# Kernel optimization log

Hardware: AMD Instinct MI355X
Metric: run time of the kernel (lower is better)

Reference implementation:

```python
import jax, jax.numpy as jnp
import numpy as np

HEADS = 8

def group_conv1x1(x, w, heads):
    # x: (B, Cin, H, W); w: (Cout, Cin//heads, 1, 1) grouped 1x1 conv, no bias
    B, Cin, H, W = x.shape
    Cout = w.shape[0]
    xg = x.reshape(B, heads, Cin // heads, H * W)
    wg = w[:, :, 0, 0].reshape(heads, Cout // heads, Cin // heads)
    out = jnp.einsum('hoc,bhcl->bhol', wg, xg)
    return out.reshape(B, Cout, H, W)

def sine_pe(d_model, length):
    # standard transformer sin/cos encoding, laid out as (d_model, length)
    pos = jnp.arange(length, dtype=jnp.float32)
    i = jnp.arange(0, d_model, 2, dtype=jnp.float32)
    div = jnp.exp(-(jnp.log(10000.0)) * i / d_model)
    ang = div[:, None] * pos[None, :]            # (d/2, L)
    pe = jnp.zeros((d_model, length), dtype=jnp.float32)
    pe = pe.at[0::2].set(jnp.sin(ang)).at[1::2].set(jnp.cos(ang))
    return pe

def setup_inputs() -> dict:
    key = jax.random.key(0)
    k0, k1, k2, k3 = jax.random.split(key, 4)
    B, Cin, H, W = 16, 256, 32, 32
    Cout, heads = 256, HEADS
    fan_out = Cout  # kaiming_normal fan_out for 1x1 conv = Cout*1*1
    std = np.sqrt(2.0 / fan_out)
    x = jax.random.normal(k0, (B, Cin, H, W), dtype=jnp.float32)
    wq = jax.random.normal(k1, (Cout, Cin // heads, 1, 1), dtype=jnp.float32) * std
    wk = jax.random.normal(k2, (Cout, Cin // heads, 1, 1), dtype=jnp.float32) * std
    wv = jax.random.normal(k3, (Cout, Cin // heads, 1, 1), dtype=jnp.float32) * std
    return {"x": x, "wq": wq, "wk": wk, "wv": wv}

def reference(x, wq, wk, wv):
    B, Cin, H, W = x.shape
    Cout = wq.shape[0]
    heads = HEADS
    dh = Cout // heads
    L = H * W

    q = group_conv1x1(x, wq, heads)              # (B, Cout, H, W)
    k = group_conv1x1(x, wk, heads)
    v = group_conv1x1(x, wv, heads)

    # sine positional encoding added to keys over flattened spatial positions
    k = k.reshape(B, Cout, L) + sine_pe(Cout, L)[None]

    q = q.reshape(B, heads, dh, L)               # (B, h, dh, L)
    k = k.reshape(B, heads, dh, L)
    v = v.reshape(B, heads, dh, L)

    scores = jnp.einsum('bhdq,bhdk->bhqk', q, k)  # (B, h, L, L) -- no sqrt(d) scaling, as in source
    attn = jax.nn.softmax(scores, axis=-1)
    out = jnp.einsum('bhqk,bhdk->bhdq', attn, v)  # (B, h, dh, L)
    return out.reshape(B, Cout, H, W)
```

## Files before the change

### kernel.cpp

```cpp
#include <hip/hip_runtime.h>

#define LL   1024
#define LOG2E 1.44269504088896340736f
#define SMEM_BYTES (131072 + 10240 + 32)

typedef unsigned int       uint;
typedef unsigned short     ushort;
typedef unsigned long long ull;

typedef __attribute__((ext_vector_type(8)))  __bf16          bf16x8;
typedef __attribute__((ext_vector_type(8)))  unsigned short  u16x8;
typedef __attribute__((ext_vector_type(4)))  unsigned short  u16x4;
typedef __attribute__((ext_vector_type(2)))  uint            ui32x2;
typedef __attribute__((ext_vector_type(4)))  uint            ui32x4;
typedef __attribute__((ext_vector_type(4)))  float           f32x4;
typedef __attribute__((ext_vector_type(16))) float           f32x16;

static __device__ __forceinline__ ushort f2bf(float f){
  union {float f; uint u;} v; v.f = f;
  uint u = v.u + 0x7fffu + ((v.u >> 16) & 1u);
  return (ushort)(u >> 16);
}
static __device__ __forceinline__ uint pack2(float a, float b){
  return (uint)f2bf(a) | ((uint)f2bf(b) << 16);
}
static __device__ __forceinline__ uint packtrunc(float a, float b){
  union {float f; uint u;} x, y; x.f = a; y.f = b;
  return __builtin_amdgcn_perm(y.u, x.u, 0x07060302u);
}
static __device__ __forceinline__ bf16x8 ld_frag(const ushort* p){
  u16x8 t = *(const u16x8*)p;
  return __builtin_bit_cast(bf16x8, t);
}
static __device__ __forceinline__ bf16x8 cvt8(const float* p){
  float4 f0 = *(const float4*)p, f1 = *(const float4*)(p + 4);
  u16x8 t;
  t[0]=f2bf(f0.x); t[1]=f2bf(f0.y); t[2]=f2bf(f0.z); t[3]=f2bf(f0.w);
  t[4]=f2bf(f1.x); t[5]=f2bf(f1.y); t[6]=f2bf(f1.z); t[7]=f2bf(f1.w);
  return __builtin_bit_cast(bf16x8, t);
}

static __device__ __forceinline__ void attn_tile(
    f32x16& O, float& rs, bf16x8 q0, bf16x8 q1,
    bf16x8 k00, bf16x8 k01, bf16x8 k10, bf16x8 k11,
    bf16x8 v0, bf16x8 v1, bf16x8 v2, bf16x8 v3, int h)
{
  f32x16 zz = {};
  f32x16 st0 = __builtin_amdgcn_mfma_f32_32x32x16_bf16(k00, q0, zz,  0,0,0);
  st0        = __builtin_amdgcn_mfma_f32_32x32x16_bf16(k01, q1, st0, 0,0,0);
  f32x16 st1 = __builtin_amdgcn_mfma_f32_32x32x16_bf16(k10, q0, zz,  0,0,0);
  st1        = __builtin_amdgcn_mfma_f32_32x32x16_bf16(k11, q1, st1, 0,0,0);

  uint pr0[8], pr1[8];
  #pragma unroll
  for (int zi = 0; zi < 8; ++zi){
    float a0 = __builtin_amdgcn_exp2f(st0[2*zi]);
    float a1 = __builtin_amdgcn_exp2f(st0[2*zi+1]);
    float b0 = __builtin_amdgcn_exp2f(st1[2*zi]);
    float b1 = __builtin_amdgcn_exp2f(st1[2*zi+1]);
    rs += (a0 + a1) + (b0 + b1);
    pr0[zi] = packtrunc(a0, a1);
    pr1[zi] = packtrunc(b0, b1);
  }
  const bf16x8 vv[4] = {v0, v1, v2, v3};
  #pragma unroll
  for (int c = 0; c < 4; ++c){
    const uint* pr = (c < 2) ? pr0 : pr1;
    const int g0 = 4*(c & 1);
    uint s0 = h ? pr[g0+0] : pr[g0+2];
    uint s1 = h ? pr[g0+1] : pr[g0+3];
    uint r0 = (uint)__shfl_xor((int)s0, 32);
    uint r1 = (uint)__shfl_xor((int)s1, 32);
    ui32x4 pb;
    pb[0] = h ? r0 : pr[g0+0];
    pb[1] = h ? r1 : pr[g0+1];
    pb[2] = h ? pr[g0+2] : r0;
    pb[3] = h ? pr[g0+3] : r1;
    O = __builtin_amdgcn_mfma_f32_32x32x16_bf16(
          vv[c], __builtin_bit_cast(bf16x8, pb), O, 0,0,0);
  }
}

__global__ __launch_bounds__(512, 1) void fused_kernel(
    const void* __restrict__ xr,
    const void* __restrict__ wqr,
    const void* __restrict__ wkr,
    const void* __restrict__ wvr,
    void* __restrict__ out)
{
  extern __shared__ __align__(16) char smem[];
  ushort* Ks = (ushort*)smem;
  ushort* Vs = Ks + 32768;
  uint (*xsd)[20] = (uint (*)[20])(Vs + 32768);
  int* cnt = (int*)(smem + 131072 + 10240);

  const int bh   = blockIdx.x;
  const int qh   = blockIdx.y;
  const int tid  = threadIdx.x;
  const int wave = tid >> 6;
  const int lane = tid & 63;
  const int l16  = lane & 15;
  const int quad = lane >> 4;
  const int q32  = lane & 31;
  const int h    = lane >> 5;

  bool is_bf;
  {
    uint w = ((const uint*)xr)[tid & 255];
    uint e = (w >> 7) & 0xFFu;
    ull b = __ballot((e >= 118u) && (e <= 132u));
    if (lane == 0) cnt[wave] = __popcll(b);
    __syncthreads();
    int s = 0;
    #pragma unroll
    for (int i = 0; i < 8; ++i) s += cnt[i];
    is_bf = s > 256;
  }

  bf16x8 bwk[2], bwv[2], aq[2];
  #pragma unroll
  for (int nh = 0; nh < 2; ++nh){
    const int row = (bh & 7)*32 + nh*16 + l16;
    if (is_bf){
      bwk[nh] = ld_frag((const ushort*)wkr + (size_t)row*32 + quad*8);
      bwv[nh] = ld_frag((const ushort*)wvr + (size_t)row*32 + quad*8);
    } else {
      bwk[nh] = cvt8((const float*)wkr + (size_t)row*32 + quad*8);
      bwv[nh] = cvt8((const float*)wvr + (size_t)row*32 + quad*8);
    }
  }
  {
    const int row = (bh & 7)*32 + q32;
    if (is_bf){
      aq[0] = ld_frag((const ushort*)wqr + (size_t)row*32 + h*8);
      aq[1] = ld_frag((const ushort*)wqr + (size_t)row*32 + 16 + h*8);
    } else {
      aq[0] = cvt8((const float*)wqr + (size_t)row*32 + h*8);
      aq[1] = cvt8((const float*)wqr + (size_t)row*32 + 16 + h*8);
    }
  }

  const int myoc = 4*qh + (wave >> 1);
  bf16x8 bq[2][2];

  for (int lc = 0; lc < 8; ++lc){
    if (lc) __syncthreads();
    {
      const int cp = tid & 15, lg = tid >> 4;
      const size_t rb = (size_t)(bh*32 + 2*cp)*LL + (size_t)lc*128 + lg*4;
      uint dw[4];
      if (is_bf){
        u16x4 e = *(const u16x4*)((const ushort*)xr + rb);
        u16x4 o = *(const u16x4*)((const ushort*)xr + rb + LL);
        #pragma unroll
        for (int j = 0; j < 4; ++j) dw[j] = (uint)e[j] | ((uint)o[j] << 16);
      } else {
        const float* xf = (const float*)xr;
        float4 e0 = *(const float4*)(xf + rb);
        float4 o0 = *(const float4*)(xf + rb + LL);
        dw[0]=pack2(e0.x,o0.x); dw[1]=pack2(e0.y,o0.y);
        dw[2]=pack2(e0.z,o0.z); dw[3]=pack2(e0.w,o0.w);
      }
      #pragma unroll
      for (int j = 0; j < 4; ++j) xsd[lg*4 + j][cp] = dw[j];
    }
    __syncthreads();

    bf16x8 ax = __builtin_bit_cast(bf16x8,
                  *(const ui32x4*)&xsd[wave*16 + l16][quad*4]);

    const f32x4 z = {0.f,0.f,0.f,0.f};
    f32x4 dk[2], dv[2];
    #pragma unroll
    for (int nh = 0; nh < 2; ++nh){
      dk[nh] = __builtin_amdgcn_mfma_f32_16x16x32_bf16(bwk[nh], ax, z, 0,0,0);
      dv[nh] = __builtin_amdgcn_mfma_f32_16x16x32_bf16(ax, bwv[nh], z, 0,0,0);
    }

    {
      const int kl = lc*128 + wave*16 + l16;
      const int kbase = (kl >> 6)*2048 + ((kl >> 5) & 1)*1024
                      + (quad >> 1)*256 + (kl & 31)*8 + (quad & 1)*4;
      #pragma unroll
      for (int nh = 0; nh < 2; ++nh){
        const int d0 = nh*16 + quad*4;
        const int c0 = (bh & 7)*32 + d0;
        const float fa = __expf(-0.03597789207f * (float)c0);
        const float fb = __expf(-0.03597789207f * (float)(c0 + 2));
        const float aa = fa * (float)kl, ab = fb * (float)kl;
        const float k0 = (dk[nh][0] + __sinf(aa)) * LOG2E;
        const float k1 = (dk[nh][1] + __cosf(aa)) * LOG2E;
        const float k2 = (dk[nh][2] + __sinf(ab)) * LOG2E;
        const float k3 = (dk[nh][3] + __cosf(ab)) * LOG2E;
        ui32x2 ww = { pack2(k0, k1), pack2(k2, k3) };
        *(ui32x2*)&Ks[kbase + nh*512] = ww;
      }
    }
    {
      const int vl = lc*128 + wave*16 + quad*4;
      const int vbase = (vl >> 6)*2048 + (wave & 3)*512
                      + (quad >> 1)*256 + (quad & 1)*4;
      #pragma unroll
      for (int nh = 0; nh < 2; ++nh){
        ui32x2 ww = { pack2(dv[nh][0], dv[nh][1]),
                      pack2(dv[nh][2], dv[nh][3]) };
        *(ui32x2*)&Vs[vbase + (nh*16 + l16)*8] = ww;
      }
    }

    if (lc == myoc){
      const int xbase = (wave & 1)*64;
      #pragma unroll
      for (int qt2 = 0; qt2 < 2; ++qt2){
        const int xrow = xbase + qt2*32 + q32;
        bf16x8 bxl = __builtin_bit_cast(bf16x8, *(const ui32x4*)&xsd[xrow][h*4]);
        bf16x8 bxh = __builtin_bit_cast(bf16x8, *(const ui32x4*)&xsd[xrow][8 + h*4]);
        f32x16 zz = {};
        f32x16 dq = __builtin_amdgcn_mfma_f32_32x32x16_bf16(aq[0], bxl, zz, 0,0,0);
        dq        = __builtin_amdgcn_mfma_f32_32x32x16_bf16(aq[1], bxh, dq, 0,0,0);
        uint prq[8];
        #pragma unroll
        for (int zi = 0; zi < 8; ++zi) prq[zi] = pack2(dq[2*zi], dq[2*zi+1]);
        #pragma unroll
        for (int hf = 0; hf < 2; ++hf){
          const int g0 = 4*hf;
          uint s0 = h ? prq[g0+0] : prq[g0+2];
          uint s1 = h ? prq[g0+1] : prq[g0+3];
          uint r0 = (uint)__shfl_xor((int)s0, 32);
          uint r1 = (uint)__shfl_xor((int)s1, 32);
          ui32x4 pb;
          pb[0] = h ? r0 : prq[g0+0];
          pb[1] = h ? r1 : prq[g0+1];
          pb[2] = h ? prq[g0+2] : r0;
          pb[3] = h ? prq[g0+3] : r1;
          bq[qt2][hf] = __builtin_bit_cast(bf16x8, pb);
        }
      }
    }
  }
  __syncthreads();

  const ushort* kb = Ks + h*256 + q32*8;
  const ushort* vb = Vs + h*256 + q32*8;

  f32x16 O0 = {}, O1 = {};
  float rs0 = 0.f, rs1 = 0.f;

  for (int kt = 0; kt < 16; ++kt){
    const ushort* kp = kb + kt*2048;
    const ushort* vp = vb + kt*2048;
    bf16x8 k00 = ld_frag(kp);
    bf16x8 k01 = ld_frag(kp + 512);
    bf16x8 k10 = ld_frag(kp + 1024);
    bf16x8 k11 = ld_frag(kp + 1536);
    bf16x8 v0  = ld_frag(vp);
    bf16x8 v1  = ld_frag(vp + 512);
    bf16x8 v2  = ld_frag(vp + 1024);
    bf16x8 v3  = ld_frag(vp + 1536);
    attn_tile(O0, rs0, bq[0][0], bq[0][1], k00,k01,k10,k11, v0,v1,v2,v3, h);
    attn_tile(O1, rs1, bq[1][0], bq[1][1], k00,k01,k10,k11, v0,v1,v2,v3, h);
  }

  rs0 += __shfl_xor(rs0, 32);
  rs1 += __shfl_xor(rs1, 32);
  const float inv0 = 1.f / rs0, inv1 = 1.f / rs1;

  const int qg0 = qh*512 + wave*64 + q32;
  #pragma unroll
  for (int reg = 0; reg < 16; ++reg){
    const int d = (reg & 3) + 8*(reg >> 2) + 4*h;
    const size_t o0 = ((size_t)(bh*32 + d))*LL + qg0;
    if (is_bf){
      ((ushort*)out)[o0]      = f2bf(O0[reg] * inv0);
      ((ushort*)out)[o0 + 32] = f2bf(O1[reg] * inv1);
    } else {
      ((float*)out)[o0]      = O0[reg] * inv0;
      ((float*)out)[o0 + 32] = O1[reg] * inv1;
    }
  }
}

extern "C" void kernel_launch(void* const* d_in, const int* in_sizes, int n_in,
                              void* d_out, int out_size, void* d_ws, size_t ws_size,
                              hipStream_t stream) {
  (void)d_ws; (void)ws_size; (void)in_sizes; (void)n_in; (void)out_size;
  static bool inited = false;
  if (!inited){
    hipFuncSetAttribute(reinterpret_cast<const void*>(fused_kernel),
                        hipFuncAttributeMaxDynamicSharedMemorySize, SMEM_BYTES);
    inited = true;
  }
  fused_kernel<<<dim3(128, 2), 512, SMEM_BYTES, stream>>>(
      d_in[0], d_in[1], d_in[2], d_in[3], d_out);
}
```

Before: 105.5 us.

## Double-buffer x staging, prefetch K/V fragments, use permlane32 swap

Double-buffers the x staging tile in shared memory and issues the global loads for the next chunk before computing on the current one, which removes one barrier per iteration. The attention loop now loads the next tile's K/V fragments from LDS into registers one iteration ahead. The lane-half exchange moves from shfl_xor with selects to v_permlane32_swap, the PE frequency exps are hoisted out of the loop, and the row-sum is split across independent accumulators. In exchange it uses more registers and twice the LDS for the x buffer, which may affect the schedule.

New measurement: 102.7 us. -2.6%, faster.

```diff
diff --git a/kernel.cpp b/kernel.cpp
--- a/kernel.cpp
+++ b/kernel.cpp
@@ -2,7 +2,7 @@
 
 #define LL   1024
 #define LOG2E 1.44269504088896340736f
-#define SMEM_BYTES (131072 + 10240 + 32)
+#define SMEM_BYTES (131072 + 20480 + 32)
 
 typedef unsigned int       uint;
 typedef unsigned short     ushort;
@@ -40,44 +40,44 @@
   return __builtin_bit_cast(bf16x8, t);
 }
 
+static __device__ __forceinline__ void plane32_swap(uint& a, uint& b){
+  asm("v_permlane32_swap_b32 %0, %1" : "+v"(a), "+v"(b));
+}
+
 static __device__ __forceinline__ void attn_tile(
     f32x16& O, float& rs, bf16x8 q0, bf16x8 q1,
-    bf16x8 k00, bf16x8 k01, bf16x8 k10, bf16x8 k11,
-    bf16x8 v0, bf16x8 v1, bf16x8 v2, bf16x8 v3, int h)
+    const bf16x8* kf, const bf16x8* vf)
 {
   f32x16 zz = {};
-  f32x16 st0 = __builtin_amdgcn_mfma_f32_32x32x16_bf16(k00, q0, zz,  0,0,0);
-  st0        = __builtin_amdgcn_mfma_f32_32x32x16_bf16(k01, q1, st0, 0,0,0);
-  f32x16 st1 = __builtin_amdgcn_mfma_f32_32x32x16_bf16(k10, q0, zz,  0,0,0);
-  st1        = __builtin_amdgcn_mfma_f32_32x32x16_bf16(k11, q1, st1, 0,0,0);
+  f32x16 st0 = __builtin_amdgcn_mfma_f32_32x32x16_bf16(kf[0], q0, zz,  0,0,0);
+  st0        = __builtin_amdgcn_mfma_f32_32x32x16_bf16(kf[1], q1, st0, 0,0,0);
+  f32x16 st1 = __builtin_amdgcn_mfma_f32_32x32x16_bf16(kf[2], q0, zz,  0,0,0);
+  st1        = __builtin_amdgcn_mfma_f32_32x32x16_bf16(kf[3], q1, st1, 0,0,0);
 
   uint pr0[8], pr1[8];
+  float s0 = 0.f, s1 = 0.f, s2 = 0.f, s3 = 0.f;
   #pragma unroll
   for (int zi = 0; zi < 8; ++zi){
     float a0 = __builtin_amdgcn_exp2f(st0[2*zi]);
     float a1 = __builtin_amdgcn_exp2f(st0[2*zi+1]);
     float b0 = __builtin_amdgcn_exp2f(st1[2*zi]);
     float b1 = __builtin_amdgcn_exp2f(st1[2*zi+1]);
-    rs += (a0 + a1) + (b0 + b1);
+    s0 += a0; s1 += a1; s2 += b0; s3 += b1;
     pr0[zi] = packtrunc(a0, a1);
     pr1[zi] = packtrunc(b0, b1);
   }
-  const bf16x8 vv[4] = {v0, v1, v2, v3};
+  rs += (s0 + s1) + (s2 + s3);
+
   #pragma unroll
   for (int c = 0; c < 4; ++c){
     const uint* pr = (c < 2) ? pr0 : pr1;
     const int g0 = 4*(c & 1);
-    uint s0 = h ? pr[g0+0] : pr[g0+2];
-    uint s1 = h ? pr[g0+1] : pr[g0+3];
-    uint r0 = (uint)__shfl_xor((int)s0, 32);
-    uint r1 = (uint)__shfl_xor((int)s1, 32);
-    ui32x4 pb;
-    pb[0] = h ? r0 : pr[g0+0];
-    pb[1] = h ? r1 : pr[g0+1];
-    pb[2] = h ? pr[g0+2] : r0;
-    pb[3] = h ? pr[g0+3] : r1;
+    uint p0 = pr[g0+0], p1 = pr[g0+1], p2 = pr[g0+2], p3 = pr[g0+3];
+    plane32_swap(p0, p2);
+    plane32_swap(p1, p3);
+    ui32x4 pb; pb[0]=p0; pb[1]=p1; pb[2]=p2; pb[3]=p3;
     O = __builtin_amdgcn_mfma_f32_32x32x16_bf16(
-          vv[c], __builtin_bit_cast(bf16x8, pb), O, 0,0,0);
+          vf[c], __builtin_bit_cast(bf16x8, pb), O, 0,0,0);
   }
 }
 
@@ -91,8 +91,8 @@
   extern __shared__ __align__(16) char smem[];
   ushort* Ks = (ushort*)smem;
   ushort* Vs = Ks + 32768;
-  uint (*xsd)[20] = (uint (*)[20])(Vs + 32768);
-  int* cnt = (int*)(smem + 131072 + 10240);
+  uint (*xbuf)[20] = (uint (*)[20])(Vs + 32768);
+  int* cnt = (int*)(smem + 131072 + 20480);
 
   const int bh   = blockIdx.x;
   const int qh   = blockIdx.y;
@@ -140,15 +140,44 @@
     }
   }
 
+  float fA[2], fB[2];
+  #pragma unroll
+  for (int nh = 0; nh < 2; ++nh){
+    const int c0 = (bh & 7)*32 + nh*16 + quad*4;
+    fA[nh] = __expf(-0.03597789207f * (float)c0);
+    fB[nh] = __expf(-0.03597789207f * (float)(c0 + 2));
+  }
+
   const int myoc = 4*qh + (wave >> 1);
   bf16x8 bq[2][2];
 
+  const int cp = tid & 15, lg = tid >> 4;
+
+  uint dw[4];
+  {
+    const size_t rb = (size_t)(bh*32 + 2*cp)*LL + lg*4;
+    if (is_bf){
+      u16x4 e = *(const u16x4*)((const ushort*)xr + rb);
+      u16x4 o = *(const u16x4*)((const ushort*)xr + rb + LL);
+      #pragma unroll
+      for (int j = 0; j < 4; ++j) dw[j] = (uint)e[j] | ((uint)o[j] << 16);
+    } else {
+      const float* xf = (const float*)xr;
+      float4 e0 = *(const float4*)(xf + rb);
+      float4 o0 = *(const float4*)(xf + rb + LL);
+      dw[0]=pack2(e0.x,o0.x); dw[1]=pack2(e0.y,o0.y);
+      dw[2]=pack2(e0.z,o0.z); dw[3]=pack2(e0.w,o0.w);
+    }
+  }
+
   for (int lc = 0; lc < 8; ++lc){
-    if (lc) __syncthreads();
-    {
-      const int cp = tid & 15, lg = tid >> 4;
-      const size_t rb = (size_t)(bh*32 + 2*cp)*LL + (size_t)lc*128 + lg*4;
-      uint dw[4];
+    uint (*xs)[20] = xbuf + (lc & 1)*128;
+    #pragma unroll
+    for (int j = 0; j < 4; ++j) xs[lg*4 + j][cp] = dw[j];
+    __syncthreads();
+
+    if (lc < 7){
+      const size_t rb = (size_t)(bh*32 + 2*cp)*LL + (size_t)(lc+1)*128 + lg*4;
       if (is_bf){
         u16x4 e = *(const u16x4*)((const ushort*)xr + rb);
         u16x4 o = *(const u16x4*)((const ushort*)xr + rb + LL);
@@ -161,13 +190,10 @@
         dw[0]=pack2(e0.x,o0.x); dw[1]=pack2(e0.y,o0.y);
         dw[2]=pack2(e0.z,o0.z); dw[3]=pack2(e0.w,o0.w);
       }
-      #pragma unroll
-      for (int j = 0; j < 4; ++j) xsd[lg*4 + j][cp] = dw[j];
-    }
-    __syncthreads();
+    }
 
     bf16x8 ax = __builtin_bit_cast(bf16x8,
-                  *(const ui32x4*)&xsd[wave*16 + l16][quad*4]);
+                  *(const ui32x4*)&xs[wave*16 + l16][quad*4]);
 
     const f32x4 z = {0.f,0.f,0.f,0.f};
     f32x4 dk[2], dv[2];
@@ -183,11 +209,7 @@
                       + (quad >> 1)*256 + (kl & 31)*8 + (quad & 1)*4;
       #pragma unroll
       for (int nh = 0; nh < 2; ++nh){
-        const int d0 = nh*16 + quad*4;
-        const int c0 = (bh & 7)*32 + d0;
-        const float fa = __expf(-0.03597789207f * (float)c0);
-        const float fb = __expf(-0.03597789207f * (float)(c0 + 2));
-        const float aa = fa * (float)kl, ab = fb * (float)kl;
+        const float aa = fA[nh] * (float)kl, ab = fB[nh] * (float)kl;
         const float k0 = (dk[nh][0] + __sinf(aa)) * LOG2E;
         const float k1 = (dk[nh][1] + __cosf(aa)) * LOG2E;
         const float k2 = (dk[nh][2] + __sinf(ab)) * LOG2E;
@@ -213,8 +235,8 @@
       #pragma unroll
       for (int qt2 = 0; qt2 < 2; ++qt2){
         const int xrow = xbase + qt2*32 + q32;
-        bf16x8 bxl = __builtin_bit_cast(bf16x8, *(const ui32x4*)&xsd[xrow][h*4]);
-        bf16x8 bxh = __builtin_bit_cast(bf16x8, *(const ui32x4*)&xsd[xrow][8 + h*4]);
+        bf16x8 bxl = __builtin_bit_cast(bf16x8, *(const ui32x4*)&xs[xrow][h*4]);
+        bf16x8 bxh = __builtin_bit_cast(bf16x8, *(const ui32x4*)&xs[xrow][8 + h*4]);
         f32x16 zz = {};
         f32x16 dq = __builtin_amdgcn_mfma_f32_32x32x16_bf16(aq[0], bxl, zz, 0,0,0);
         dq        = __builtin_amdgcn_mfma_f32_32x32x16_bf16(aq[1], bxh, dq, 0,0,0);
@@ -224,15 +246,10 @@
         #pragma unroll
         for (int hf = 0; hf < 2; ++hf){
           const int g0 = 4*hf;
-          uint s0 = h ? prq[g0+0] : prq[g0+2];
-          uint s1 = h ? prq[g0+1] : prq[g0+3];
-          uint r0 = (uint)__shfl_xor((int)s0, 32);
-          uint r1 = (uint)__shfl_xor((int)s1, 32);
-          ui32x4 pb;
-          pb[0] = h ? r0 : prq[g0+0];
-          pb[1] = h ? r1 : prq[g0+1];
-          pb[2] = h ? prq[g0+2] : r0;
-          pb[3] = h ? prq[g0+3] : r1;
+          uint p0 = prq[g0+0], p1 = prq[g0+1], p2 = prq[g0+2], p3 = prq[g0+3];
+          plane32_swap(p0, p2);
+          plane32_swap(p1, p3);
+          ui32x4 pb; pb[0]=p0; pb[1]=p1; pb[2]=p2; pb[3]=p3;
           bq[qt2][hf] = __builtin_bit_cast(bf16x8, pb);
         }
       }
@@ -246,19 +263,25 @@
   f32x16 O0 = {}, O1 = {};
   float rs0 = 0.f, rs1 = 0.f;
 
+  bf16x8 kf[4], vf[4];
+  #pragma unroll
+  for (int i = 0; i < 4; ++i){
+    kf[i] = ld_frag(kb + i*512);
+    vf[i] = ld_frag(vb + i*512);
+  }
+
   for (int kt = 0; kt < 16; ++kt){
-    const ushort* kp = kb + kt*2048;
-    const ushort* vp = vb + kt*2048;
-    bf16x8 k00 = ld_frag(kp);
-    bf16x8 k01 = ld_frag(kp + 512);
-    bf16x8 k10 = ld_frag(kp + 1024);
-    bf16x8 k11 = ld_frag(kp + 1536);
-    bf16x8 v0  = ld_frag(vp);
-    bf16x8 v1  = ld_frag(vp + 512);
-    bf16x8 v2  = ld_frag(vp + 1024);
-    bf16x8 v3  = ld_frag(vp + 1536);
-    attn_tile(O0, rs0, bq[0][0], bq[0][1], k00,k01,k10,k11, v0,v1,v2,v3, h);
-    attn_tile(O1, rs1, bq[1][0], bq[1][1], k00,k01,k10,k11, v0,v1,v2,v3, h);
+    const int nkt = (kt + 1) & 15;
+    bf16x8 nk[4], nv[4];
+    #pragma unroll
+    for (int i = 0; i < 4; ++i){
+      nk[i] = ld_frag(kb + nkt*2048 + i*512);
+      nv[i] = ld_frag(vb + nkt*2048 + i*512);
+    }
+    attn_tile(O0, rs0, bq[0][0], bq[0][1], kf, vf);
+    attn_tile(O1, rs1, bq[1][0], bq[1][1], kf, vf);
+    #pragma unroll
+    for (int i = 0; i < 4; ++i){ kf[i] = nk[i]; vf[i] = nv[i]; }
   }
 
   rs0 += __shfl_xor(rs0, 32);
```
